# Kernel tuning notes

Hardware: AMD Instinct MI355X
Metric: run time of the kernel (lower is better)

The kernel has to match this reference:

```python
import jax, jax.numpy as jnp
import numpy as np

B, T, HID = 2, 2048, 2048
NH, NKV, HD = 16, 8, 128
CACHE_LEN = 2048
SCALE = HD ** -0.5


def _rope_tables(t, d2, theta=10000.0):
    inv = 1.0 / (theta ** (np.arange(0, d2, dtype=np.float32) / d2))
    ang = np.arange(t, dtype=np.float32)[:, None] * inv[None, :]
    return jnp.asarray(np.cos(ang)), jnp.asarray(np.sin(ang))


def setup_inputs() -> dict:
    key = jax.random.key(0)
    k1, k2, k3, k4, k5 = jax.random.split(key, 5)
    cos, sin = _rope_tables(T, HD // 2)
    # causal additive mask, Gemma-style large negative
    neg = jnp.asarray(-2.3819763e38, dtype=jnp.float32)
    causal = jnp.where(jnp.tril(jnp.ones((T, CACHE_LEN), dtype=bool)), 0.0, neg)
    return {
        "hidden_states": jax.random.normal(k1, (B, T, HID), jnp.float32) * 0.02,
        "freqs_cos": cos,
        "freqs_sin": sin,
        "k_cache": jnp.zeros((B, CACHE_LEN, NKV, HD), jnp.float32),
        "v_cache": jnp.zeros((B, CACHE_LEN, NKV, HD), jnp.float32),
        "mask": causal[None, None, :, :],
        "w_qkv": jax.random.normal(k2, ((NH + 2 * NKV) * HD, HID), jnp.float32) * (HID ** -0.5),
        "w_o": jax.random.normal(k3, (HID, NH * HD), jnp.float32) * ((NH * HD) ** -0.5),
        "kv_write_indices": jnp.arange(T, dtype=jnp.int64),
    }


def apply_rope(x, cos, sin):
    # x: [B, T, H, D]; cos/sin: [T, D/2]. Matches Gemma apply_rotary_emb
    # (complex mul on (x1, x2) halves, output concat[real, imag]).
    xf = x.astype(jnp.float32)
    d2 = xf.shape[-1] // 2
    x1, x2 = xf[..., :d2], xf[..., d2:]
    c = cos[None, :, None, :]
    s = sin[None, :, None, :]
    out = jnp.concatenate([x1 * c - x2 * s, x1 * s + x2 * c], axis=-1)
    return out.astype(x.dtype)


def reference(hidden_states, freqs_cos, freqs_sin, k_cache, v_cache, mask, w_qkv, w_o, kv_write_indices):
    b, t, _ = hidden_states.shape
    qkv = hidden_states @ w_qkv.T  # [B, T, (NH+2NKV)*HD]
    q_size, kv_size = NH * HD, NKV * HD
    xq = qkv[..., :q_size].reshape(b, t, NH, HD)
    xk = qkv[..., q_size:q_size + kv_size].reshape(b, t, NKV, HD)
    xv = qkv[..., q_size + kv_size:].reshape(b, t, NKV, HD)
    xq = apply_rope(xq, freqs_cos, freqs_sin)
    xk = apply_rope(xk, freqs_cos, freqs_sin)
    # KV cache write (index_copy_ along seq dim)
    k_cache = k_cache.at[:, kv_write_indices].set(xk)
    v_cache = v_cache.at[:, kv_write_indices].set(xv)
    # GQA: repeat_interleave kv heads along head dim
    n_rep = NH // NKV
    key = jnp.repeat(k_cache, n_rep, axis=2)  # [B, S, NH, HD]
    value = jnp.repeat(v_cache, n_rep, axis=2)
    scores = jnp.einsum("bqhd,bkhd->bhqk", xq, key) * SCALE
    scores = scores + mask
    probs = jax.nn.softmax(scores.astype(jnp.float32), axis=-1).astype(xq.dtype)
    out = jnp.einsum("bhqk,bkhd->bqhd", probs, value)
    out = out.reshape(b, t, NH * HD)
    return out @ w_o.T
```

## Files before the change

### kernel.cpp

```cpp
#include <hip/hip_runtime.h>
#include <stdint.h>

#define T_SEQ 2048
#define NHEADS 16
#define NKVH 8
#define HDIM 128
#define SCALE_F 0.08838834764831845f

typedef __bf16 bf16_t;
typedef __attribute__((ext_vector_type(8))) __bf16 bf16x8;
typedef __attribute__((ext_vector_type(4))) float f32x4;
typedef __attribute__((ext_vector_type(2))) unsigned int u32x2;
typedef __attribute__((ext_vector_type(4))) unsigned int u32x4;

__device__ __forceinline__ void gload_lds16(const bf16_t* g, bf16_t* l) {
  __builtin_amdgcn_global_load_lds(
      (const __attribute__((address_space(1))) void*)g,
      (__attribute__((address_space(3))) void*)l, 16, 0, 0);
}

__global__ __launch_bounds__(256) void cvt_bf16(const float* __restrict__ s,
                                                bf16_t* __restrict__ d, int n8) {
  const int i = blockIdx.x * 256 + threadIdx.x;
  if (i >= n8) return;
  const float4* sp = (const float4*)s + (size_t)i * 2;
  const float4 a = sp[0], b = sp[1];
  union { bf16_t e[8]; u32x4 v; } u;
  u.e[0] = (bf16_t)a.x; u.e[1] = (bf16_t)a.y; u.e[2] = (bf16_t)a.z; u.e[3] = (bf16_t)a.w;
  u.e[4] = (bf16_t)b.x; u.e[5] = (bf16_t)b.y; u.e[6] = (bf16_t)b.z; u.e[7] = (bf16_t)b.w;
  *((u32x4*)d + i) = u.v;
}

template <typename OutT>
__global__ __launch_bounds__(256) void gemm_bt(const bf16_t* __restrict__ A,
                                               const bf16_t* __restrict__ B,
                                               OutT* __restrict__ C,
                                               int M, int N, int K) {
  __shared__ bf16_t sA[128 * 32];
  __shared__ bf16_t sB[128 * 32];
  const int tid = threadIdx.x;
  const int wave = tid >> 6;
  const int lane = tid & 63;
  const int q = lane & 15, g = lane >> 4;
  const int wm = wave >> 1, wn = wave & 1;
  const int bn = blockIdx.x, bm = blockIdx.y;
  const size_t Ks = (size_t)K;
  f32x4 acc[4][4] = {};
  const int srow = tid >> 2;
  const int scol = (tid & 3) << 3;
  for (int ks = 0; ks < K; ks += 32) {
    __syncthreads();
#pragma unroll
    for (int it = 0; it < 2; ++it) {
      const int row = it * 64 + srow;
      gload_lds16(A + (size_t)(bm * 128 + row) * Ks + ks + scol,
                  sA + it * 2048 + wave * 512);
      gload_lds16(B + (size_t)(bn * 128 + row) * Ks + ks + scol,
                  sB + it * 2048 + wave * 512);
    }
    __syncthreads();
    bf16x8 af[4], bfr[4];
#pragma unroll
    for (int m = 0; m < 4; ++m)
      af[m] = *(const bf16x8*)(sA + (wm * 64 + m * 16 + q) * 32 + g * 8);
#pragma unroll
    for (int n = 0; n < 4; ++n)
      bfr[n] = *(const bf16x8*)(sB + (wn * 64 + n * 16 + q) * 32 + g * 8);
#pragma unroll
    for (int m = 0; m < 4; ++m)
#pragma unroll
      for (int n = 0; n < 4; ++n)
        acc[m][n] = __builtin_amdgcn_mfma_f32_16x16x32_bf16(af[m], bfr[n], acc[m][n], 0, 0, 0);
  }
#pragma unroll
  for (int m = 0; m < 4; ++m) {
    const int row0 = bm * 128 + wm * 64 + m * 16 + g * 4;
#pragma unroll
    for (int n = 0; n < 4; ++n) {
      const int col = bn * 128 + wn * 64 + n * 16 + q;
#pragma unroll
      for (int i = 0; i < 4; ++i)
        C[(size_t)(row0 + i) * N + col] = (OutT)acc[m][n][i];
    }
  }
}

__global__ __launch_bounds__(256) void rope_inplace(bf16_t* __restrict__ qkv,
    const float* __restrict__ fc, const float* __restrict__ fs) {
  const int tok = blockIdx.x;
  const int t = tok & 2047;
  const int tid = threadIdx.x;
  const size_t base = (size_t)tok * 4096;
#pragma unroll
  for (int r = 0; r < 4; ++r) {
    const int p = tid + 256 * r;
    const int hh = p >> 6, d = p & 63;
    const float x1 = (float)qkv[base + hh * 128 + d];
    const float x2 = (float)qkv[base + hh * 128 + d + 64];
    const float c = fc[t * 64 + d], s = fs[t * 64 + d];
    qkv[base + hh * 128 + d]      = (bf16_t)((x1 * c - x2 * s) * SCALE_F);
    qkv[base + hh * 128 + d + 64] = (bf16_t)((x1 * s + x2 * c) * SCALE_F);
  }
#pragma unroll
  for (int r = 0; r < 2; ++r) {
    const int p = tid + 256 * r;
    const int hh = p >> 6, d = p & 63;
    const size_t o = base + 2048 + hh * 128 + d;
    const float x1 = (float)qkv[o];
    const float x2 = (float)qkv[o + 64];
    const float c = fc[t * 64 + d], s = fs[t * 64 + d];
    qkv[o]      = (bf16_t)(x1 * c - x2 * s);
    qkv[o + 64] = (bf16_t)(x1 * s + x2 * c);
  }
}

__global__ __launch_bounds__(256) void attn_fwd(const bf16_t* __restrict__ qkv,
                                                bf16_t* __restrict__ O) {
  __shared__ bf16_t sK[32 * 128];
  __shared__ bf16_t sVT[128 * 32];
  const int tid = threadIdx.x, w = tid >> 6, lane = tid & 63;
  const int q = lane & 15, g = lane >> 4;
  const int qb = blockIdx.x, hh = blockIdx.y, b = blockIdx.z;
  const int kvh = hh >> 1;
  const int q_glob = qb * 64 + w * 16 + q;
  const bf16_t* Qbase = qkv + ((size_t)(b * T_SEQ) + qb * 64 + w * 16 + q) * 4096 + hh * 128;
  bf16x8 qf[4];
#pragma unroll
  for (int kc = 0; kc < 4; ++kc)
    qf[kc] = *(const bf16x8*)(Qbase + kc * 32 + g * 8);
  f32x4 o_[8] = {};
  float mx = -1e30f, lsum = 0.f;
  const int ntiles = qb * 2 + 2;
  for (int tt = 0; tt < ntiles; ++tt) {
    const int kt = tt * 32;
    __syncthreads();
    {
      const int kr = tid >> 4;
      const int ce = (tid & 15) * 8;
#pragma unroll
      for (int it = 0; it < 2; ++it) {
        const int krow = kr + it * 16;
        const bf16_t* Krow = qkv + ((size_t)(b * T_SEQ) + kt + krow) * 4096 + 2048 + kvh * 128;
        const u32x4 kv_ = *(const u32x4*)(Krow + ce);
        *(u32x4*)((char*)sK + krow * 256 + ((ce * 2) ^ ((krow & 7) << 4))) = kv_;
        const u32x4 vv = *(const u32x4*)(Krow + 1024 + ce);
        union { u32x4 v; bf16_t e[8]; } vs; vs.v = vv;
#pragma unroll
        for (int e2 = 0; e2 < 8; ++e2) {
          const int d = ce + e2;
          const int sb = (d >> 3) & 7;
          sVT[d * 32 + ((((krow >> 2) ^ sb) << 2) | (krow & 3))] = vs.e[e2];
        }
      }
    }
    __syncthreads();
    if (kt <= qb * 64 + w * 16 + 15) {
      f32x4 st0 = {}, st1 = {};
#pragma unroll
      for (int kc = 0; kc < 4; ++kc) {
        const int r1 = 16 + q;
        const bf16x8 k0 = *(const bf16x8*)((const char*)sK + q * 256 + ((kc * 64 + g * 16) ^ ((q & 7) << 4)));
        const bf16x8 k1 = *(const bf16x8*)((const char*)sK + r1 * 256 + ((kc * 64 + g * 16) ^ ((r1 & 7) << 4)));
        st0 = __builtin_amdgcn_mfma_f32_16x16x32_bf16(k0, qf[kc], st0, 0, 0, 0);
        st1 = __builtin_amdgcn_mfma_f32_16x16x32_bf16(k1, qf[kc], st1, 0, 0, 0);
      }
      float sv[8];
#pragma unroll
      for (int i = 0; i < 4; ++i) {
        sv[i]     = (kt + g * 4 + i      <= q_glob) ? st0[i] : -1e30f;
        sv[4 + i] = (kt + 16 + g * 4 + i <= q_glob) ? st1[i] : -1e30f;
      }
      float pm = sv[0];
#pragma unroll
      for (int j = 1; j < 8; ++j) pm = fmaxf(pm, sv[j]);
      pm = fmaxf(pm, __shfl_xor(pm, 16));
      pm = fmaxf(pm, __shfl_xor(pm, 32));
      const float mnew = fmaxf(mx, pm);
      const float sf = __expf(mx - mnew);
      float p[8], ps = 0.f;
#pragma unroll
      for (int j = 0; j < 8; ++j) { p[j] = __expf(sv[j] - mnew); ps += p[j]; }
      ps += __shfl_xor(ps, 16);
      ps += __shfl_xor(ps, 32);
      lsum = lsum * sf + ps;
      mx = mnew;
#pragma unroll
      for (int m = 0; m < 8; ++m) o_[m] *= sf;
      union { bf16_t e[8]; bf16x8 v; } pu;
#pragma unroll
      for (int j = 0; j < 8; ++j) pu.e[j] = (bf16_t)p[j];
#pragma unroll
      for (int m = 0; m < 8; ++m) {
        const int d = m * 16 + q;
        const int sb = (d >> 3) & 7;
        union { u32x2 h[2]; bf16x8 v; } vu;
        vu.h[0] = *(const u32x2*)(sVT + d * 32 + ((g ^ sb) << 2));
        vu.h[1] = *(const u32x2*)(sVT + d * 32 + (((4 + g) ^ sb) << 2));
        o_[m] = __builtin_amdgcn_mfma_f32_16x16x32_bf16(vu.v, pu.v, o_[m], 0, 0, 0);
      }
    }
  }
  const float rl = 1.0f / lsum;
  const size_t ob = ((size_t)b * T_SEQ + qb * 64 + w * 16 + q) * (NHEADS * HDIM) + hh * HDIM;
#pragma unroll
  for (int m = 0; m < 8; ++m) {
    union { bf16_t e[4]; u32x2 v; } ou;
#pragma unroll
    for (int i = 0; i < 4; ++i) ou.e[i] = (bf16_t)(o_[m][i] * rl);
    *(u32x2*)(O + ob + m * 16 + g * 4) = ou.v;
  }
}

extern "C" void kernel_launch(void* const* d_in, const int* in_sizes, int n_in,
                              void* d_out, int out_size, void* d_ws, size_t ws_size,
                              hipStream_t stream) {
  (void)in_sizes; (void)n_in; (void)out_size; (void)ws_size;
  const float* hidden = (const float*)d_in[0];
  const float* fcos   = (const float*)d_in[1];
  const float* fsin   = (const float*)d_in[2];
  const float* w_qkv  = (const float*)d_in[6];
  const float* w_o    = (const float*)d_in[7];

  bf16_t* hb  = (bf16_t*)d_ws;
  bf16_t* wqb = hb + (size_t)8388608;
  bf16_t* qkv = (bf16_t*)d_ws + (size_t)16777216;
  bf16_t* att = hb;
  bf16_t* wob = wqb;
  float*  out = (float*)d_out;

  cvt_bf16<<<dim3(4096), 256, 0, stream>>>(hidden, hb, 1048576);
  cvt_bf16<<<dim3(4096), 256, 0, stream>>>(w_qkv, wqb, 1048576);
  gemm_bt<bf16_t><<<dim3(32, 32), 256, 0, stream>>>(hb, wqb, qkv, 4096, 4096, 2048);
  rope_inplace<<<dim3(4096), 256, 0, stream>>>(qkv, fcos, fsin);
  attn_fwd<<<dim3(32, NHEADS, 2), 256, 0, stream>>>(qkv, att);
  cvt_bf16<<<dim3(2048), 256, 0, stream>>>(w_o, wob, 524288);
  gemm_bt<float><<<dim3(16, 32), 256, 0, stream>>>(att, wob, out, 4096, 2048, 2048);
}
```

Baseline: 516.4 us.

## Pipeline attention KV tiles with register prefetch, double-buffered LDS, and causal pairing

Rewrites the attention kernel to process 64-key tiles with double-buffered shared memory. The next tile's K/V global loads are prefetched into registers while the current tile is computed, so each tile needs one barrier instead of two. Each block now handles a pair of query blocks (qb and 31-qb) to balance causal work, which halves the grid. The kernel also masks only on the diagonal tile and skips the rescale when the running max grows by 8 or less. This trades extra registers and LDS (launch bounds 256,2) for less stall time and better load balance.

```diff
diff --git a/kernel.cpp b/kernel.cpp
--- a/kernel.cpp
+++ b/kernel.cpp
@@ -114,100 +114,149 @@
   }
 }
 
-__global__ __launch_bounds__(256) void attn_fwd(const bf16_t* __restrict__ qkv,
-                                                bf16_t* __restrict__ O) {
-  __shared__ bf16_t sK[32 * 128];
-  __shared__ bf16_t sVT[128 * 32];
+struct Stage { u32x4 k[4]; u32x4 v[4]; };
+
+__global__ __launch_bounds__(256, 2) void attn_fwd(const bf16_t* __restrict__ qkv,
+                                                   bf16_t* __restrict__ O) {
+  __shared__ bf16_t sK[2][8192];
+  __shared__ bf16_t sV[2][8192];
   const int tid = threadIdx.x, w = tid >> 6, lane = tid & 63;
   const int q = lane & 15, g = lane >> 4;
-  const int qb = blockIdx.x, hh = blockIdx.y, b = blockIdx.z;
+  const int hh = blockIdx.y, b = blockIdx.z;
   const int kvh = hh >> 1;
-  const int q_glob = qb * 64 + w * 16 + q;
-  const bf16_t* Qbase = qkv + ((size_t)(b * T_SEQ) + qb * 64 + w * 16 + q) * 4096 + hh * 128;
-  bf16x8 qf[4];
-#pragma unroll
-  for (int kc = 0; kc < 4; ++kc)
-    qf[kc] = *(const bf16x8*)(Qbase + kc * 32 + g * 8);
-  f32x4 o_[8] = {};
-  float mx = -1e30f, lsum = 0.f;
-  const int ntiles = qb * 2 + 2;
-  for (int tt = 0; tt < ntiles; ++tt) {
-    const int kt = tt * 32;
-    __syncthreads();
-    {
-      const int kr = tid >> 4;
-      const int ce = (tid & 15) * 8;
-#pragma unroll
-      for (int it = 0; it < 2; ++it) {
-        const int krow = kr + it * 16;
-        const bf16_t* Krow = qkv + ((size_t)(b * T_SEQ) + kt + krow) * 4096 + 2048 + kvh * 128;
-        const u32x4 kv_ = *(const u32x4*)(Krow + ce);
-        *(u32x4*)((char*)sK + krow * 256 + ((ce * 2) ^ ((krow & 7) << 4))) = kv_;
-        const u32x4 vv = *(const u32x4*)(Krow + 1024 + ce);
-        union { u32x4 v; bf16_t e[8]; } vs; vs.v = vv;
+  const bf16_t* kvb = qkv + (size_t)(b * T_SEQ) * 4096 + 2048 + kvh * 128;
+
+  auto issue_loads = [&](int kt, Stage& r) {
+#pragma unroll
+    for (int it = 0; it < 4; ++it) {
+      const int c = tid + 256 * it;
+      const int row = c >> 4;
+      const int ce = (c & 15) * 8;
+      const bf16_t* p = kvb + (size_t)(kt + row) * 4096 + ce;
+      r.k[it] = *(const u32x4*)p;
+      r.v[it] = *(const u32x4*)(p + 1024);
+    }
+  };
+
+#pragma unroll 1
+  for (int half = 0; half < 2; ++half) {
+    const int qb = half ? (31 - (int)blockIdx.x) : (int)blockIdx.x;
+    const int nt = qb + 1;
+    const int q_glob = qb * 64 + w * 16 + q;
+    const bf16_t* Qb = qkv + ((size_t)(b * T_SEQ) + q_glob) * 4096 + hh * 128;
+    bf16x8 qf[4];
+#pragma unroll
+    for (int kc = 0; kc < 4; ++kc)
+      qf[kc] = *(const bf16x8*)(Qb + kc * 32 + g * 8);
+    f32x4 o_[8] = {};
+    float mx = -1e30f, lsum = 0.f;
+    Stage rA, rB;
+    issue_loads(0, rA);
+
+    auto tile = [&](int t, Stage& cur, Stage& nxt) {
+      bf16_t* sKb = sK[t & 1];
+      bf16_t* sVb = sV[t & 1];
+#pragma unroll
+      for (int it = 0; it < 4; ++it) {
+        const int c = tid + 256 * it;
+        const int row = c >> 4;
+        const int ce = (c & 15) * 8;
+        *(u32x4*)((char*)sKb + row * 256 + ((ce * 2) ^ ((row & 7) << 4))) = cur.k[it];
+        bf16_t* sVg = sVb + ((row >> 5) << 12);
+        const int vrow = row & 31;
+        union { u32x4 v; bf16_t e[8]; } vs; vs.v = cur.v[it];
 #pragma unroll
         for (int e2 = 0; e2 < 8; ++e2) {
           const int d = ce + e2;
           const int sb = (d >> 3) & 7;
-          sVT[d * 32 + ((((krow >> 2) ^ sb) << 2) | (krow & 3))] = vs.e[e2];
+          sVg[d * 32 + ((((vrow >> 2) ^ sb) << 2) | (vrow & 3))] = vs.e[e2];
         }
       }
-    }
-    __syncthreads();
-    if (kt <= qb * 64 + w * 16 + 15) {
-      f32x4 st0 = {}, st1 = {};
-#pragma unroll
-      for (int kc = 0; kc < 4; ++kc) {
-        const int r1 = 16 + q;
-        const bf16x8 k0 = *(const bf16x8*)((const char*)sK + q * 256 + ((kc * 64 + g * 16) ^ ((q & 7) << 4)));
-        const bf16x8 k1 = *(const bf16x8*)((const char*)sK + r1 * 256 + ((kc * 64 + g * 16) ^ ((r1 & 7) << 4)));
-        st0 = __builtin_amdgcn_mfma_f32_16x16x32_bf16(k0, qf[kc], st0, 0, 0, 0);
-        st1 = __builtin_amdgcn_mfma_f32_16x16x32_bf16(k1, qf[kc], st1, 0, 0, 0);
-      }
-      float sv[8];
-#pragma unroll
-      for (int i = 0; i < 4; ++i) {
-        sv[i]     = (kt + g * 4 + i      <= q_glob) ? st0[i] : -1e30f;
-        sv[4 + i] = (kt + 16 + g * 4 + i <= q_glob) ? st1[i] : -1e30f;
-      }
-      float pm = sv[0];
-#pragma unroll
-      for (int j = 1; j < 8; ++j) pm = fmaxf(pm, sv[j]);
+      if (t + 1 < nt) issue_loads((t + 1) * 64, nxt);
+      asm volatile("s_waitcnt lgkmcnt(0)" ::: "memory");
+      __builtin_amdgcn_s_barrier();
+      __builtin_amdgcn_sched_barrier(0);
+      const int kt = t * 64;
+      f32x4 st[4] = {};
+#pragma unroll
+      for (int kc = 0; kc < 4; ++kc)
+#pragma unroll
+        for (int h = 0; h < 4; ++h) {
+          const int row = h * 16 + q;
+          const bf16x8 kf = *(const bf16x8*)((const char*)sKb + row * 256 +
+                                             ((kc * 64 + g * 16) ^ ((row & 7) << 4)));
+          st[h] = __builtin_amdgcn_mfma_f32_16x16x32_bf16(kf, qf[kc], st[h], 0, 0, 0);
+        }
+      float p[4][4];
+      const bool diag = (t == nt - 1);
+#pragma unroll
+      for (int h = 0; h < 4; ++h)
+#pragma unroll
+        for (int i = 0; i < 4; ++i) {
+          float v = st[h][i];
+          if (diag) v = (kt + h * 16 + g * 4 + i <= q_glob) ? v : -1e30f;
+          p[h][i] = v;
+        }
+      float pm = p[0][0];
+#pragma unroll
+      for (int h = 0; h < 4; ++h)
+#pragma unroll
+        for (int i = 0; i < 4; ++i) pm = fmaxf(pm, p[h][i]);
       pm = fmaxf(pm, __shfl_xor(pm, 16));
       pm = fmaxf(pm, __shfl_xor(pm, 32));
-      const float mnew = fmaxf(mx, pm);
-      const float sf = __expf(mx - mnew);
-      float p[8], ps = 0.f;
-#pragma unroll
-      for (int j = 0; j < 8; ++j) { p[j] = __expf(sv[j] - mnew); ps += p[j]; }
+      if (!__all(pm - mx <= 8.f)) {
+        const float mnew = fmaxf(mx, pm);
+        const float sf = __expf(mx - mnew);
+        lsum *= sf;
+#pragma unroll
+        for (int m = 0; m < 8; ++m) o_[m] *= sf;
+        mx = mnew;
+      }
+      float ps = 0.f;
+#pragma unroll
+      for (int h = 0; h < 4; ++h)
+#pragma unroll
+        for (int i = 0; i < 4; ++i) { p[h][i] = __expf(p[h][i] - mx); ps += p[h][i]; }
       ps += __shfl_xor(ps, 16);
       ps += __shfl_xor(ps, 32);
-      lsum = lsum * sf + ps;
-      mx = mnew;
-#pragma unroll
-      for (int m = 0; m < 8; ++m) o_[m] *= sf;
-      union { bf16_t e[8]; bf16x8 v; } pu;
-#pragma unroll
-      for (int j = 0; j < 8; ++j) pu.e[j] = (bf16_t)p[j];
+      lsum += ps;
+      union { bf16_t e[8]; bf16x8 v; } pu0, pu1;
+#pragma unroll
+      for (int j = 0; j < 4; ++j) {
+        pu0.e[j] = (bf16_t)p[0][j]; pu0.e[4 + j] = (bf16_t)p[1][j];
+        pu1.e[j] = (bf16_t)p[2][j]; pu1.e[4 + j] = (bf16_t)p[3][j];
+      }
+      const bf16_t* sV0 = sVb;
+      const bf16_t* sV1 = sVb + 4096;
 #pragma unroll
       for (int m = 0; m < 8; ++m) {
         const int d = m * 16 + q;
         const int sb = (d >> 3) & 7;
-        union { u32x2 h[2]; bf16x8 v; } vu;
-        vu.h[0] = *(const u32x2*)(sVT + d * 32 + ((g ^ sb) << 2));
-        vu.h[1] = *(const u32x2*)(sVT + d * 32 + (((4 + g) ^ sb) << 2));
-        o_[m] = __builtin_amdgcn_mfma_f32_16x16x32_bf16(vu.v, pu.v, o_[m], 0, 0, 0);
-      }
-    }
-  }
-  const float rl = 1.0f / lsum;
-  const size_t ob = ((size_t)b * T_SEQ + qb * 64 + w * 16 + q) * (NHEADS * HDIM) + hh * HDIM;
-#pragma unroll
-  for (int m = 0; m < 8; ++m) {
-    union { bf16_t e[4]; u32x2 v; } ou;
-#pragma unroll
-    for (int i = 0; i < 4; ++i) ou.e[i] = (bf16_t)(o_[m][i] * rl);
-    *(u32x2*)(O + ob + m * 16 + g * 4) = ou.v;
+        union { u32x2 h2[2]; bf16x8 v; } v0, v1;
+        v0.h2[0] = *(const u32x2*)(sV0 + d * 32 + ((g ^ sb) << 2));
+        v0.h2[1] = *(const u32x2*)(sV0 + d * 32 + (((4 + g) ^ sb) << 2));
+        v1.h2[0] = *(const u32x2*)(sV1 + d * 32 + ((g ^ sb) << 2));
+        v1.h2[1] = *(const u32x2*)(sV1 + d * 32 + (((4 + g) ^ sb) << 2));
+        o_[m] = __builtin_amdgcn_mfma_f32_16x16x32_bf16(v0.v, pu0.v, o_[m], 0, 0, 0);
+        o_[m] = __builtin_amdgcn_mfma_f32_16x16x32_bf16(v1.v, pu1.v, o_[m], 0, 0, 0);
+      }
+    };
+
+    int t = 0;
+    while (true) {
+      tile(t, rA, rB); if (++t == nt) break;
+      tile(t, rB, rA); if (++t == nt) break;
+    }
+    const float rl = 1.0f / lsum;
+    const size_t ob = ((size_t)b * T_SEQ + q_glob) * (NHEADS * HDIM) + hh * HDIM;
+#pragma unroll
+    for (int m = 0; m < 8; ++m) {
+      union { bf16_t e[4]; u32x2 v; } ou;
+#pragma unroll
+      for (int i = 0; i < 4; ++i) ou.e[i] = (bf16_t)(o_[m][i] * rl);
+      *(u32x2*)(O + ob + m * 16 + g * 4) = ou.v;
+    }
+    __builtin_amdgcn_s_barrier();
   }
 }
 
@@ -232,7 +281,7 @@
   cvt_bf16<<<dim3(4096), 256, 0, stream>>>(w_qkv, wqb, 1048576);
   gemm_bt<bf16_t><<<dim3(32, 32), 256, 0, stream>>>(hb, wqb, qkv, 4096, 4096, 2048);
   rope_inplace<<<dim3(4096), 256, 0, stream>>>(qkv, fcos, fsin);
-  attn_fwd<<<dim3(32, NHEADS, 2), 256, 0, stream>>>(qkv, att);
+  attn_fwd<<<dim3(16, NHEADS, 2), 256, 0, stream>>>(qkv, att);
   cvt_bf16<<<dim3(2048), 256, 0, stream>>>(w_o, wob, 524288);
   gemm_bt<float><<<dim3(16, 32), 256, 0, stream>>>(att, wob, out, 4096, 2048, 2048);
 }
```

Result: faster. 441.2 us (-14.5%).
